# Kernel optimization log

Measured on AMD Instinct MI355X. Metric: run time of the kernel, lower is better.

Reference implementation:

```python
import jax, jax.numpy as jnp
import numpy as np

BETA = 1.0  # write blending coefficient (beta in original module)


def ste(x):
    # Binarize with straight-through estimator: forward (x>0.5), backward identity.
    b = (x > 0.5).astype(x.dtype)
    return x + jax.lax.stop_gradient(b - x)


def setup_inputs() -> dict:
    key = jax.random.key(0)
    k0, k1, k2 = jax.random.split(key, 3)
    B, H, W, HID = 8, 512, 512, 64
    f0 = jax.random.uniform(k0, (B, 1, H, W), dtype=jnp.float32)
    W1 = jax.random.normal(k1, (9, HID), dtype=jnp.float32) * (1.0 / np.sqrt(9.0))
    b1 = jnp.zeros((HID,), dtype=jnp.float32)
    W2 = jax.random.normal(k2, (HID, 1), dtype=jnp.float32) * (1.0 / np.sqrt(HID))
    b2 = jnp.zeros((1,), dtype=jnp.float32)
    return {"f0": f0, "W1": W1, "b1": b1, "W2": W2, "b2": b2, "T": 16}


def reference(f0, W1, b1, W2, b2, T):
    B, _, H, Wd = f0.shape

    def step(f, _):
        f_read = ste(f)                                            # (B,1,H,W) binarized read
        pad = jnp.pad(f_read, ((0, 0), (0, 0), (1, 1), (1, 1)), mode="wrap")
        # 3x3 neighborhoods, row-major top-left -> bottom-right: (B,H,W,9)
        neigh = jnp.stack(
            [pad[:, 0, i:i + H, j:j + Wd] for i in range(3) for j in range(3)],
            axis=-1,
        )
        h = jax.nn.relu(jnp.einsum("bhwn,nk->bhwk", neigh, W1) + b1)
        logits = (jnp.einsum("bhwk,ko->bhwo", h, W2) + b2)[..., 0]  # (B,H,W)
        w_bits = ste(jax.nn.sigmoid(logits))[:, None]               # (B,1,H,W)
        f_new = (1.0 - BETA) * f + BETA * w_bits
        return f_new, f_new

    _, rest = jax.lax.scan(step, f0, None, length=T - 1)
    fields = jnp.concatenate([f0[None], rest], axis=0)  # (T,B,1,H,W)
    return fields
```

## Files before the change

kernel.cpp:

```cpp
#include <hip/hip_runtime.h>

#define HH 512
#define WW 512
#define WORDS_PER_ROW (WW / 32)
#define RO 16
#define HALO 15
#define ROWS (RO + 2 * HALO)

__global__ void build_lut(const float* __restrict__ W1, const float* __restrict__ b1,
                          const float* __restrict__ W2, const float* __restrict__ b2,
                          int hid, unsigned int* __restrict__ lut12g) {
    __shared__ unsigned int rule[512];
    int p = threadIdx.x;
    float logit = b2[0];
    for (int k = 0; k < hid; ++k) {
        float a = b1[k];
#pragma unroll
        for (int n = 0; n < 9; ++n)
            if (p & (1 << n)) a += W1[n * hid + k];
        logit += fmaxf(a, 0.0f) * W2[k];
    }
    rule[p] = (logit > 0.0f) ? 1u : 0u;
    __syncthreads();

    if (p < 256) {
        unsigned int wv = 0;
#pragma unroll
        for (int k = 0; k < 16; ++k) {
            unsigned int e = (unsigned int)p * 16u + k;
            unsigned int u = e & 15u, m = (e >> 4) & 15u, d = (e >> 8) & 15u;
            unsigned int i0 = (u & 7u) | ((m & 7u) << 3) | ((d & 7u) << 6);
            unsigned int i1 = (u >> 1) | ((m >> 1) << 3) | ((d >> 1) << 6);
            unsigned int bits = rule[i0] | (rule[i1] << 1);
            wv |= bits << (2 * k);
        }
        lut12g[p] = wv;
    }
}

__global__ __launch_bounds__(256) void init_field(const float* __restrict__ f0,
                                                  float* __restrict__ out,
                                                  unsigned long long* __restrict__ field) {
    int c = blockIdx.x * 256 + threadIdx.x;
    float v = f0[c];
    out[c] = v;
    unsigned long long m = __ballot(v > 0.5f);
    if ((threadIdx.x & 63) == 0) field[c >> 6] = m;
}

__global__ __launch_bounds__(512) void fused_steps(const unsigned int* __restrict__ field,
                                                   const unsigned int* __restrict__ lut12g,
                                                   float* __restrict__ out,
                                                   int n, int T) {
    __shared__ unsigned int lut[256];
    __shared__ unsigned int bufA[ROWS * WORDS_PER_ROW];
    __shared__ unsigned int bufB[ROWS * WORDS_PER_ROW];

    const int tid = threadIdx.x;
    const int b = blockIdx.x >> 5;
    const int r0 = (blockIdx.x & 31) * RO;
    const unsigned int* F = field + b * (HH * WORDS_PER_ROW);
    float* outb = out + (size_t)b * (HH * WW);

    if (tid < 256) lut[tid] = lut12g[tid];
    for (int i = tid; i < ROWS * WORDS_PER_ROW; i += 512) {
        int l = i >> 4, w = i & 15;
        int g = (r0 - HALO + l) & (HH - 1);
        bufA[i] = F[g * WORDS_PER_ROW + w];
    }
    __syncthreads();

    unsigned int* oldb = bufA;
    unsigned int* newb = bufB;

    for (int t = 1; t < T; ++t) {
        const int lo = t, hi = ROWS - t;
        for (int l = lo + (tid >> 4); l < hi; l += 32) {
            const int w = tid & 15;
            const int wp = (w + 15) & 15, wn = (w + 1) & 15;
            const unsigned int* Ru = oldb + (l - 1) * WORDS_PER_ROW;
            const unsigned int* Rm = oldb + l * WORDS_PER_ROW;
            const unsigned int* Rd = oldb + (l + 1) * WORDS_PER_ROW;
            unsigned long long eu = ((((unsigned long long)Ru[wn] << 32) | Ru[w]) << 1) | (Ru[wp] >> 31);
            unsigned long long em = ((((unsigned long long)Rm[wn] << 32) | Rm[w]) << 1) | (Rm[wp] >> 31);
            unsigned long long ed = ((((unsigned long long)Rd[wn] << 32) | Rd[w]) << 1) | (Rd[wp] >> 31);
            unsigned int ow = 0;
#pragma unroll
            for (int j = 0; j < 16; ++j) {
                unsigned int idx = (unsigned int)((eu >> (2 * j)) & 15ull)
                                 | ((unsigned int)((em >> (2 * j)) & 15ull) << 4)
                                 | ((unsigned int)((ed >> (2 * j)) & 15ull) << 8);
                unsigned int bits = (lut[idx >> 4] >> ((idx & 15u) * 2)) & 3u;
                ow |= bits << (2 * j);
            }
            newb[l * WORDS_PER_ROW + w] = ow;
        }
        __syncthreads();
        float* outt = outb + (size_t)t * n;
#pragma unroll
        for (int rep = 0; rep < 4; ++rep) {
            int cell = (rep * 512 + tid) * 4;
            int lr = cell >> 9;
            int col = cell & 511;
            unsigned int wv = newb[(HALO + lr) * WORDS_PER_ROW + (col >> 5)];
            unsigned int nib = (wv >> (col & 31)) & 15u;
            float4 v;
            v.x = (float)(nib & 1u);
            v.y = (float)((nib >> 1) & 1u);
            v.z = (float)((nib >> 2) & 1u);
            v.w = (float)(nib >> 3);
            *(float4*)(outt + (size_t)(r0 + lr) * WW + col) = v;
        }
        unsigned int* tmp = oldb; oldb = newb; newb = tmp;
        if (t + 1 < T) __syncthreads();
    }
}

extern "C" void kernel_launch(void* const* d_in, const int* in_sizes, int n_in,
                              void* d_out, int out_size, void* d_ws, size_t ws_size,
                              hipStream_t stream) {
    const float* f0 = (const float*)d_in[0];
    const float* W1 = (const float*)d_in[1];
    const float* b1 = (const float*)d_in[2];
    const float* W2 = (const float*)d_in[3];
    const float* b2 = (const float*)d_in[4];
    float* out = (float*)d_out;

    const int n = in_sizes[0];
    const int hid = in_sizes[2];
    const int T = out_size / n;
    const int B = n / (HH * WW);

    char* ws = (char*)d_ws;
    unsigned int* lut12 = (unsigned int*)ws;
    unsigned long long* fld = (unsigned long long*)(ws + 1024);

    build_lut<<<1, 512, 0, stream>>>(W1, b1, W2, b2, hid, lut12);
    init_field<<<n / 256, 256, 0, stream>>>(f0, out, fld);
    fused_steps<<<B * (HH / RO), 512, 0, stream>>>((const unsigned int*)fld, lut12, out, n, T);
}
```

Baseline: 67.20 us.

## Split field tiles by column halves and fold LUT build into stepping kernel

The stepping kernel now splits each 16-row tile into two column halves with a one-word halo on each side, which doubles the block count to spread work over more CUs. Every thread computes a single word per step, so the row loop is gone. The separate LUT-building kernel is removed, and each block recomputes the 512-entry rule table and the 2-bit LUT from the weights, which saves a launch and the global LUT round-trip. The trailing per-step barrier is also dropped, relying on double buffering for safety. In exchange, each block repeats the hid×9 weight evaluation and pays extra halo overhead in columns.

```diff
diff --git a/kernel.cpp b/kernel.cpp
--- a/kernel.cpp
+++ b/kernel.cpp
@@ -2,41 +2,12 @@
 
 #define HH 512
 #define WW 512
-#define WORDS_PER_ROW (WW / 32)
+#define WPR 16
 #define RO 16
 #define HALO 15
 #define ROWS (RO + 2 * HALO)
-
-__global__ void build_lut(const float* __restrict__ W1, const float* __restrict__ b1,
-                          const float* __restrict__ W2, const float* __restrict__ b2,
-                          int hid, unsigned int* __restrict__ lut12g) {
-    __shared__ unsigned int rule[512];
-    int p = threadIdx.x;
-    float logit = b2[0];
-    for (int k = 0; k < hid; ++k) {
-        float a = b1[k];
-#pragma unroll
-        for (int n = 0; n < 9; ++n)
-            if (p & (1 << n)) a += W1[n * hid + k];
-        logit += fmaxf(a, 0.0f) * W2[k];
-    }
-    rule[p] = (logit > 0.0f) ? 1u : 0u;
-    __syncthreads();
-
-    if (p < 256) {
-        unsigned int wv = 0;
-#pragma unroll
-        for (int k = 0; k < 16; ++k) {
-            unsigned int e = (unsigned int)p * 16u + k;
-            unsigned int u = e & 15u, m = (e >> 4) & 15u, d = (e >> 8) & 15u;
-            unsigned int i0 = (u & 7u) | ((m & 7u) << 3) | ((d & 7u) << 6);
-            unsigned int i1 = (u >> 1) | ((m >> 1) << 3) | ((d >> 1) << 6);
-            unsigned int bits = rule[i0] | (rule[i1] << 1);
-            wv |= bits << (2 * k);
-        }
-        lut12g[p] = wv;
-    }
-}
+#define OW 8
+#define TW 10
 
 __global__ __launch_bounds__(256) void init_field(const float* __restrict__ f0,
                                                   float* __restrict__ out,
@@ -48,71 +19,110 @@
     if ((threadIdx.x & 63) == 0) field[c >> 6] = m;
 }
 
-__global__ __launch_bounds__(512) void fused_steps(const unsigned int* __restrict__ field,
-                                                   const unsigned int* __restrict__ lut12g,
-                                                   float* __restrict__ out,
-                                                   int n, int T) {
+__global__ __launch_bounds__(512) void mega(const unsigned int* __restrict__ field,
+                                            const float* __restrict__ W1,
+                                            const float* __restrict__ b1,
+                                            const float* __restrict__ W2,
+                                            const float* __restrict__ b2,
+                                            int hid, float* __restrict__ out,
+                                            int n, int T) {
+    __shared__ unsigned int rule[512];
     __shared__ unsigned int lut[256];
-    __shared__ unsigned int bufA[ROWS * WORDS_PER_ROW];
-    __shared__ unsigned int bufB[ROWS * WORDS_PER_ROW];
+    __shared__ unsigned int bufA[ROWS * TW];
+    __shared__ unsigned int bufB[ROWS * TW];
 
     const int tid = threadIdx.x;
-    const int b = blockIdx.x >> 5;
-    const int r0 = (blockIdx.x & 31) * RO;
-    const unsigned int* F = field + b * (HH * WORDS_PER_ROW);
-    float* outb = out + (size_t)b * (HH * WW);
+    const int cg = blockIdx.x & 1;
+    const int rg = (blockIdx.x >> 1) & 31;
+    const int b  = blockIdx.x >> 6;
+    const int r0 = rg * RO;
+    const int q0 = cg * OW;
+    const int c0 = cg * (OW * 32);
 
-    if (tid < 256) lut[tid] = lut12g[tid];
-    for (int i = tid; i < ROWS * WORDS_PER_ROW; i += 512) {
-        int l = i >> 4, w = i & 15;
-        int g = (r0 - HALO + l) & (HH - 1);
-        bufA[i] = F[g * WORDS_PER_ROW + w];
+    {
+        int p = tid;
+        float logit = b2[0];
+        for (int k = 0; k < hid; ++k) {
+            float a = b1[k];
+#pragma unroll
+            for (int nn = 0; nn < 9; ++nn)
+                if (p & (1 << nn)) a += W1[nn * hid + k];
+            logit += fmaxf(a, 0.0f) * W2[k];
+        }
+        rule[p] = (logit > 0.0f) ? 1u : 0u;
+    }
+    __syncthreads();
+
+    if (tid < 256) {
+        unsigned int wv = 0;
+#pragma unroll
+        for (int k = 0; k < 16; ++k) {
+            unsigned int e = (unsigned int)tid * 16u + k;
+            unsigned int u = e & 15u, m = (e >> 4) & 15u, d = (e >> 8) & 15u;
+            unsigned int i0 = (u & 7u) | ((m & 7u) << 3) | ((d & 7u) << 6);
+            unsigned int i1 = (u >> 1) | ((m >> 1) << 3) | ((d >> 1) << 6);
+            wv |= (rule[i0] | (rule[i1] << 1)) << (2 * k);
+        }
+        lut[tid] = wv;
+    }
+
+    {
+        const unsigned int* F = field + b * (HH * WPR);
+        for (int i = tid; i < ROWS * TW; i += 512) {
+            int l = i / TW, tw = i - l * TW;
+            int g  = (r0 - HALO + l) & (HH - 1);
+            int gw = (q0 - 1 + tw) & (WPR - 1);
+            bufA[i] = F[g * WPR + gw];
+        }
     }
     __syncthreads();
 
     unsigned int* oldb = bufA;
     unsigned int* newb = bufB;
+    float* outb = out + (size_t)b * (HH * WW);
 
     for (int t = 1; t < T; ++t) {
-        const int lo = t, hi = ROWS - t;
-        for (int l = lo + (tid >> 4); l < hi; l += 32) {
-            const int w = tid & 15;
-            const int wp = (w + 15) & 15, wn = (w + 1) & 15;
-            const unsigned int* Ru = oldb + (l - 1) * WORDS_PER_ROW;
-            const unsigned int* Rm = oldb + l * WORDS_PER_ROW;
-            const unsigned int* Rd = oldb + (l + 1) * WORDS_PER_ROW;
-            unsigned long long eu = ((((unsigned long long)Ru[wn] << 32) | Ru[w]) << 1) | (Ru[wp] >> 31);
-            unsigned long long em = ((((unsigned long long)Rm[wn] << 32) | Rm[w]) << 1) | (Rm[wp] >> 31);
-            unsigned long long ed = ((((unsigned long long)Rd[wn] << 32) | Rd[w]) << 1) | (Rd[wp] >> 31);
+        const int hi = ROWS - t;
+        const int lq = tid / TW;
+        const int w  = tid - lq * TW;
+        const int l  = t + lq;
+        if (l < hi) {
+            const unsigned int* Ru = oldb + (l - 1) * TW;
+            const unsigned int* Rm = oldb + l * TW;
+            const unsigned int* Rd = oldb + (l + 1) * TW;
+            const int wl = (w == 0) ? 0 : w - 1;
+            const int wn = (w == TW - 1) ? TW - 1 : w + 1;
+            unsigned long long eu = ((((unsigned long long)Ru[wn] << 32) | Ru[w]) << 1) | (Ru[wl] >> 31);
+            unsigned long long em = ((((unsigned long long)Rm[wn] << 32) | Rm[w]) << 1) | (Rm[wl] >> 31);
+            unsigned long long ed = ((((unsigned long long)Rd[wn] << 32) | Rd[w]) << 1) | (Rd[wl] >> 31);
             unsigned int ow = 0;
 #pragma unroll
             for (int j = 0; j < 16; ++j) {
                 unsigned int idx = (unsigned int)((eu >> (2 * j)) & 15ull)
                                  | ((unsigned int)((em >> (2 * j)) & 15ull) << 4)
                                  | ((unsigned int)((ed >> (2 * j)) & 15ull) << 8);
-                unsigned int bits = (lut[idx >> 4] >> ((idx & 15u) * 2)) & 3u;
-                ow |= bits << (2 * j);
+                ow |= ((lut[idx >> 4] >> ((idx & 15u) * 2)) & 3u) << (2 * j);
             }
-            newb[l * WORDS_PER_ROW + w] = ow;
+            newb[l * TW + w] = ow;
         }
         __syncthreads();
+
         float* outt = outb + (size_t)t * n;
 #pragma unroll
-        for (int rep = 0; rep < 4; ++rep) {
+        for (int rep = 0; rep < 2; ++rep) {
             int cell = (rep * 512 + tid) * 4;
-            int lr = cell >> 9;
-            int col = cell & 511;
-            unsigned int wv = newb[(HALO + lr) * WORDS_PER_ROW + (col >> 5)];
+            int lr  = cell >> 8;
+            int col = cell & 255;
+            unsigned int wv = newb[(HALO + lr) * TW + 1 + (col >> 5)];
             unsigned int nib = (wv >> (col & 31)) & 15u;
             float4 v;
             v.x = (float)(nib & 1u);
             v.y = (float)((nib >> 1) & 1u);
             v.z = (float)((nib >> 2) & 1u);
             v.w = (float)(nib >> 3);
-            *(float4*)(outt + (size_t)(r0 + lr) * WW + col) = v;
+            *(float4*)(outt + (size_t)(r0 + lr) * WW + c0 + col) = v;
         }
         unsigned int* tmp = oldb; oldb = newb; newb = tmp;
-        if (t + 1 < T) __syncthreads();
     }
 }
 
@@ -131,11 +141,9 @@
     const int T = out_size / n;
     const int B = n / (HH * WW);
 
-    char* ws = (char*)d_ws;
-    unsigned int* lut12 = (unsigned int*)ws;
-    unsigned long long* fld = (unsigned long long*)(ws + 1024);
+    unsigned long long* fld = (unsigned long long*)d_ws;
 
-    build_lut<<<1, 512, 0, stream>>>(W1, b1, W2, b2, hid, lut12);
     init_field<<<n / 256, 256, 0, stream>>>(f0, out, fld);
-    fused_steps<<<B * (HH / RO), 512, 0, stream>>>((const unsigned int*)fld, lut12, out, n, T);
+    mega<<<B * (HH / RO) * 2, 512, 0, stream>>>((const unsigned int*)fld,
+                                                W1, b1, W2, b2, hid, out, n, T);
 }
```

Result: no change. 66.69 us (-0.8%).
